# Kernel tuning notes

Measured on AMD Instinct MI355X. Metric: run time of the kernel, lower is better.

Reference implementation:

```python
import jax, jax.numpy as jnp
import numpy as np

# ---- config mirroring init kwargs ----
D_MODEL = 512
NUM_DIRS = 8
QUANTILES = (0.1, 0.5, 0.9)
POLY_ORDER = 2
BETA_INIT = 0.5
HEAD_WIDTH = 16
SOFTSORT_C = 0.5
SOFTSORT_ALPHA = 0.5
FEAT_IN = NUM_DIRS * (len(QUANTILES) + POLY_ORDER + 1)  # 48


def _legendre_basis(T, order, dtype):
    t = jnp.linspace(-1.0, 1.0, T, dtype=dtype)
    P = [jnp.ones_like(t)]
    if order >= 1:
        P.append(t)
    for n in range(1, order):
        P.append(((2 * n + 1) * t * P[n] - n * P[n - 1]) / (n + 1))
    B = jnp.stack(P[:order + 1], axis=0)
    return B / jnp.sqrt(jnp.maximum(jnp.sum(B * B, axis=1, keepdims=True), 1e-6))


def _isotonic_nonincreasing(y):
    #   v_i = min_{s<=i} max_{t>=i} mean(y[s..t])
    T = y.shape[0]
    c = jnp.concatenate([jnp.zeros((1,), y.dtype), jnp.cumsum(y)])
    s_idx = jnp.arange(T)[:, None]
    t_idx = jnp.arange(T)[None, :]
    length = jnp.maximum(t_idx - s_idx + 1, 1).astype(y.dtype)
    A = (c[t_idx + 1] - c[s_idx]) / length                 # mean over [s, t]
    A = jnp.where(t_idx >= s_idx, A, -jnp.inf)
    R = jax.lax.cummax(A, axis=1, reverse=True)            # R[s,i] = max_{t>=i} A[s,t]
    R = jnp.where(s_idx <= t_idx, R, jnp.inf)
    V = jax.lax.cummin(R, axis=0)                          # V[i,i] = min_{s<=i} R[s,i]
    return jnp.diagonal(V)


def _soft_sort_ascending(vals, reg):
    # Blondel et al. fast-soft-sort with L2 regularization.
    # Descending soft-sort: rho/reg - isotonic_nonincreasing(rho/reg - sort_desc(theta))
    # Ascending = -soft_sort_desc(-vals).
    L, T = vals.shape
    theta = -vals
    s = jnp.sort(theta, axis=-1)[:, ::-1]                  # descending
    rho = jnp.arange(T, 0, -1, dtype=vals.dtype) / jnp.asarray(reg, vals.dtype)
    v = jax.vmap(_isotonic_nonincreasing)(rho[None, :] - s)
    return -(rho[None, :] - v)


def setup_inputs() -> dict:
    key = jax.random.key(0)
    ks = jax.random.split(key, 6)
    B, T, N, D = 2, 128, 128, D_MODEL
    x = jax.random.normal(ks[0], (B, T, N, D), dtype=jnp.float32)
    valid_mask = jnp.ones((B, T, N), dtype=jnp.float32)
    # proj: Linear(D, K, bias=False), kaiming-uniform-ish init
    bound = 1.0 / np.sqrt(D)
    W_proj = jax.random.uniform(ks[1], (NUM_DIRS, D), jnp.float32, -bound, bound)
    # additive head: per-feature Linear(1,width) -> GELU -> Linear(width,D,no bias)
    W1 = jax.random.uniform(ks[2], (FEAT_IN, HEAD_WIDTH), jnp.float32, -1.0, 1.0)
    b1 = jax.random.uniform(ks[3], (FEAT_IN, HEAD_WIDTH), jnp.float32, -1.0, 1.0)
    bw = 1.0 / np.sqrt(HEAD_WIDTH)
    W2 = jax.random.uniform(ks[4], (FEAT_IN, HEAD_WIDTH, D_MODEL), jnp.float32, -bw, bw)
    beta = jnp.full((D_MODEL,), BETA_INIT, dtype=jnp.float32)
    return {"x": x, "valid_mask": valid_mask, "W_proj": W_proj,
            "W1": W1, "b1": b1, "W2": W2, "beta": beta}


def reference(x, valid_mask, W_proj, W1, b1, W2, beta):
    B, T, N, D = x.shape
    K = W_proj.shape[0]
    # orthonormalize projection (done in-place under no_grad in torch -> straight-through)
    Q, _ = jnp.linalg.qr(W_proj.T)                          # [D, K]
    W_eff = W_proj + jax.lax.stop_gradient(Q.T - W_proj)
    U = W_eff.T                                             # [D, K]

    v = jnp.einsum('btnd,dk->btnk', x, U) * valid_mask[..., None]
    v_bnkt = jnp.transpose(v, (0, 2, 3, 1))                 # [B, N, K, T]

    reg = max(1e-3, SOFTSORT_C * float(T) ** (-SOFTSORT_ALPHA))
    ss = _soft_sort_ascending(v_bnkt.reshape(-1, T), reg)   # [L, T]

    levels = jnp.asarray(QUANTILES, x.dtype)
    pos = jnp.clip(levels, 0.0, 1.0) * (T - 1)
    lo = jnp.clip(jnp.floor(pos).astype(jnp.int32), 0, T - 1)
    hi = jnp.clip(jnp.ceil(pos).astype(jnp.int32), 0, T - 1)
    w = pos - lo.astype(x.dtype)
    qv = ((1.0 - w) * ss[:, lo] + w * ss[:, hi]).reshape(B, N, K, -1)

    Bmat = _legendre_basis(T, POLY_ORDER, x.dtype)          # [P+1, T]
    coeff = jnp.einsum('bnkt,pt->bnkp', v_bnkt, Bmat)

    feats = jnp.concatenate([qv, coeff], axis=-1).reshape(B, N, -1)  # [B, N, F]
    hmid = jax.nn.gelu(feats[..., None] * W1 + b1, approximate=False)  # [B, N, F, width]
    parts = jnp.einsum('bnfw,fwd->bnfd', hmid, W2)          # [B, N, F, D]
    y = parts.sum(axis=2)                                   # [B, N, D]

    beta_eff = jax.nn.sigmoid(beta)
    y_btnd = jnp.broadcast_to(y[:, None], (B, T, N, D))
    h = x + beta_eff * y_btnd
    vm = valid_mask[..., None]
    h = vm * h + (1.0 - vm) * x

    num = jnp.mean(jnp.sqrt(jnp.sum((beta_eff * y_btnd) ** 2, axis=-1)))
    den = jnp.maximum(jnp.mean(jnp.sqrt(jnp.sum(x * x, axis=-1))), 1e-9)
    r = jax.lax.stop_gradient(num / den)
    # per-feature energy: contributions are constant over T -> factor T inside sqrt
    sq = jnp.sum((beta_eff * parts) ** 2, axis=(1, 3))       # [B, F]
    energy = jnp.sqrt(jnp.asarray(T, x.dtype) * sq)
    r_feat = jax.lax.stop_gradient(jnp.mean(energy, axis=0) / den)
    return h, r, r_feat
```

## Files before the change

kernel.cpp:

```cpp
#include <hip/hip_runtime.h>
#include <hip/hip_bf16.h>
#include <math.h>

#define OFF_BEFF  0
#define OFF_B2    512
#define OFF_LB    1024
#define OFF_U     1408
#define OFF_FEATS 5504
#define OFF_DENP  17792
#define OFF_NUMP  18816
#define OFF_SQP   19072
#define OFF_V     31360
#define OFF_Y     293504
#define OFF_YP    424576
#define WS_TOTAL  1473152

__device__ __align__(16) float g_ws[WS_TOTAL];

static __device__ __forceinline__ float wred64(float v){
  #pragma unroll
  for (int m = 32; m >= 1; m >>= 1) v += __shfl_xor(v, m, 64);
  return v;
}

__global__ __launch_bounds__(256) void k1_prep(const float* __restrict__ Wp,
                                               const float* __restrict__ beta){
  int tid = threadIdx.x;
  __shared__ float p1s[128], p2s[128], nrm[2];
  for (int d = tid; d < 512; d += 256){
    float b = beta[d];
    float s = 1.0f/(1.0f + expf(-b));
    g_ws[OFF_BEFF + d] = s;
    g_ws[OFF_B2 + d] = s*s;
  }
  if (tid < 128){
    float t = -1.0f + 2.0f*(float)tid/127.0f;
    p1s[tid] = t;
    p2s[tid] = 0.5f*(3.0f*t*t - 1.0f);
  }
  __syncthreads();
  if (tid == 0){
    float a = 0, b = 0;
    for (int i = 0; i < 128; i++){ a += p1s[i]*p1s[i]; b += p2s[i]*p2s[i]; }
    nrm[0] = sqrtf(fmaxf(a, 1e-6f));
    nrm[1] = sqrtf(fmaxf(b, 1e-6f));
  }
  __syncthreads();
  if (tid < 128){
    g_ws[OFF_LB + 0*128 + tid] = 1.0f/sqrtf(128.0f);
    g_ws[OFF_LB + 1*128 + tid] = p1s[tid]/nrm[0];
    g_ws[OFF_LB + 2*128 + tid] = p2s[tid]/nrm[1];
  }
  if (tid < 64){
    int l = tid;
    float A[8][8], Q[8][8], tau[8];
    #pragma unroll
    for (int c = 0; c < 8; c++)
      #pragma unroll
      for (int p = 0; p < 8; p++)
        A[c][p] = Wp[c*512 + p*64 + l];
    #pragma unroll
    for (int j = 0; j < 8; j++){
      float alpha = __shfl(A[j][0], j, 64);
      float ssq = 0.0f;
      #pragma unroll
      for (int p = 0; p < 8; p++){
        bool live = (p > 0) || (l > j);
        float v = A[j][p];
        ssq += live ? v*v : 0.0f;
      }
      ssq = wred64(ssq);
      float tj, scale;
      if (ssq == 0.0f){ tj = 0.0f; scale = 0.0f; }
      else {
        float bta = -copysignf(sqrtf(alpha*alpha + ssq), alpha);
        tj = (bta - alpha)/bta;
        scale = 1.0f/(alpha - bta);
      }
      tau[j] = tj;
      #pragma unroll
      for (int p = 0; p < 8; p++){
        int row = p*64 + l;
        float v = A[j][p]*scale;
        A[j][p] = (row < j) ? 0.0f : (row == j ? 1.0f : v);
      }
      #pragma unroll
      for (int c = j+1; c < 8; c++){
        float d = 0.0f;
        #pragma unroll
        for (int p = 0; p < 8; p++) d += A[c][p]*A[j][p];
        d = wred64(d)*tj;
        #pragma unroll
        for (int p = 0; p < 8; p++) A[c][p] -= d*A[j][p];
      }
    }
    #pragma unroll
    for (int c = 0; c < 8; c++)
      #pragma unroll
      for (int p = 0; p < 8; p++)
        Q[c][p] = (p == 0 && l == c) ? 1.0f : 0.0f;
    #pragma unroll
    for (int j = 7; j >= 0; j--){
      #pragma unroll
      for (int c = 0; c < 8; c++){
        float d = 0.0f;
        #pragma unroll
        for (int p = 0; p < 8; p++) d += Q[c][p]*A[j][p];
        d = wred64(d)*tau[j];
        #pragma unroll
        for (int p = 0; p < 8; p++) Q[c][p] -= d*A[j][p];
      }
    }
    #pragma unroll
    for (int c = 0; c < 8; c++)
      #pragma unroll
      for (int p = 0; p < 8; p++)
        g_ws[OFF_U + c*512 + p*64 + l] = Q[c][p];
  }
}

__global__ __launch_bounds__(256) void k2_proj(const float* __restrict__ x,
                                               const float* __restrict__ vmask){
  int tid = threadIdx.x;
  int l = tid & 63, wv = tid >> 6;
  int g = blockIdx.x*4 + wv;
  __shared__ float denw[4];
  float u[8][8];
  #pragma unroll
  for (int k = 0; k < 8; k++)
    #pragma unroll
    for (int e = 0; e < 8; e++)
      u[k][e] = g_ws[OFF_U + k*512 + l*8 + e];
  float denpart = 0.0f;
  for (int rr = 0; rr < 8; rr++){
    int row = g*8 + rr;
    const float* xr = x + (size_t)row*512 + l*8;
    float4 xa = *(const float4*)xr;
    float4 xb = *(const float4*)(xr + 4);
    float xe[8] = {xa.x, xa.y, xa.z, xa.w, xb.x, xb.y, xb.z, xb.w};
    float acc[8];
    float sq = 0.0f;
    #pragma unroll
    for (int k = 0; k < 8; k++){
      float a = 0.0f;
      #pragma unroll
      for (int e = 0; e < 8; e++) a += xe[e]*u[k][e];
      acc[k] = a;
    }
    #pragma unroll
    for (int e = 0; e < 8; e++) sq += xe[e]*xe[e];
    #pragma unroll
    for (int k = 0; k < 8; k++) acc[k] = wred64(acc[k]);
    sq = wred64(sq);
    if (l == 0){
      float vm = vmask[row];
      int b = row >> 14, t = (row >> 7) & 127, n = row & 127;
      int bn = b*128 + n;
      float* vg = g_ws + OFF_V + bn*1024 + t;
      #pragma unroll
      for (int k = 0; k < 8; k++) vg[k*128] = acc[k]*vm;
      denpart += sqrtf(sq);
    }
  }
  if (l == 0) denw[wv] = denpart;
  __syncthreads();
  if (tid == 0) g_ws[OFF_DENP + blockIdx.x] = denw[0]+denw[1]+denw[2]+denw[3];
}

__global__ __launch_bounds__(256) void k3_sortfeat(){
  int tid = threadIdx.x;
  int l = tid & 63, wv = tid >> 6;
  int rho = blockIdx.x*4 + wv;
  __shared__ float orig[4][128], srt[4][128], Bl[384];
  __shared__ float pS[4][128];
  __shared__ int   pC[4][128];
  for (int i = tid; i < 384; i += 256) Bl[i] = g_ws[OFF_LB + i];
  const float* vr = g_ws + OFF_V + rho*128;
  orig[wv][2*l]   = vr[2*l];
  orig[wv][2*l+1] = vr[2*l+1];
  srt[wv][2*l] = 0.0f; srt[wv][2*l+1] = 0.0f;
  __syncthreads();
  float c0, c1, c2;
  {
    float a = orig[wv][2*l], b = orig[wv][2*l+1];
    c0 = a*Bl[2*l]       + b*Bl[2*l+1];
    c1 = a*Bl[128+2*l]   + b*Bl[128+2*l+1];
    c2 = a*Bl[256+2*l]   + b*Bl[256+2*l+1];
  }
  c0 = wred64(c0); c1 = wred64(c1); c2 = wred64(c2);
  float e0 = orig[wv][2*l], e1 = orig[wv][2*l+1];
  int r0 = 0, r1 = 0;
  for (int j = 0; j < 128; j++){
    float vj = orig[wv][j];
    r0 += (vj < e0) || (vj == e0 && j < 2*l);
    r1 += (vj < e1) || (vj == e1 && j < 2*l+1);
  }
  srt[wv][r0] = e0;
  srt[wv][r1] = e1;
  __syncthreads();
  const float rinv = 22.627416997969522f;
  bool v0 = (srt[wv][2*l+1] - srt[wv][2*l] > rinv);
  bool v1 = (2*l + 2 < 128) ? (srt[wv][2*l+2] - srt[wv][2*l+1] > rinv) : false;
  if (__any(v0 || v1)){
    if (l == 0){
      int top = -1;
      for (int i = 0; i < 128; i++){
        float y = (float)(128 - i)*rinv + srt[wv][i];
        top++; pS[wv][top] = y; pC[wv][top] = 1;
        while (top > 0 &&
               pS[wv][top]*(float)pC[wv][top-1] > pS[wv][top-1]*(float)pC[wv][top]){
          pS[wv][top-1] += pS[wv][top];
          pC[wv][top-1] += pC[wv][top];
          top--;
        }
      }
      int i = 0;
      for (int blk = 0; blk <= top; blk++){
        float m = pS[wv][blk]/(float)pC[wv][blk];
        for (int c = 0; c < pC[wv][blk]; c++){
          srt[wv][i] = m - (float)(128 - i)*rinv;
          i++;
        }
      }
    }
  }
  if (l == 0){
    int bn = rho >> 3, k = rho & 7;
    float* fb = g_ws + OFF_FEATS + bn*48 + k*6;
    float w0 = 0.1f*127.0f - 12.0f;
    float w1 = 0.5f*127.0f - 63.0f;
    float w2 = 0.9f*127.0f - 114.0f;
    fb[0] = (1.0f - w0)*srt[wv][12]  + w0*srt[wv][13];
    fb[1] = (1.0f - w1)*srt[wv][63]  + w1*srt[wv][64];
    fb[2] = (1.0f - w2)*srt[wv][114] + w2*srt[wv][115];
    fb[3] = c0; fb[4] = c1; fb[5] = c2;
  }
}

__global__ __launch_bounds__(512) void k4a_head(const float* __restrict__ W1,
                                                const float* __restrict__ b1,
                                                const float* __restrict__ W2){
  int blk = blockIdx.x;
  int s   = blk & 7;
  int bnp = blk >> 3;
  int bn0 = bnp*2, bn1 = bn0 + 1;
  int tid = threadIdx.x;
  int l = tid & 63, wv = tid >> 6;
  __shared__ float hl0[96], hl1[96];
  __shared__ float sq[8][12];
  if (tid < 192){
    int which = tid >= 96;
    int i = which ? tid - 96 : tid;
    int f = s*6 + (i >> 4);
    int k = f*16 + (i & 15);
    int bn = which ? bn1 : bn0;
    float a = g_ws[OFF_FEATS + bn*48 + f]*W1[k] + b1[k];
    float g = 0.5f*a*(1.0f + erff(a*0.70710678118654752f));
    if (which) hl1[i] = g; else hl0[i] = g;
  }
  __syncthreads();
  int d = tid;
  float b2 = g_ws[OFF_B2 + d];
  float y0 = 0.0f, y1 = 0.0f;
  const float* w2base = W2 + (size_t)(s*96)*512 + d;
  #pragma unroll
  for (int fl_ = 0; fl_ < 6; fl_++){
    float p0 = 0.0f, p1 = 0.0f;
    #pragma unroll
    for (int w = 0; w < 16; w++){
      float w2 = w2base[(size_t)(fl_*16 + w)*512];
      p0 += hl0[fl_*16 + w]*w2;
      p1 += hl1[fl_*16 + w]*w2;
    }
    y0 += p0; y1 += p1;
    float e0 = wred64(p0*p0*b2);
    float e1 = wred64(p1*p1*b2);
    if (l == 0){ sq[wv][fl_*2] = e0; sq[wv][fl_*2 + 1] = e1; }
  }
  g_ws[OFF_YP + (size_t)(bn0*8 + s)*512 + d] = y0;
  g_ws[OFF_YP + (size_t)(bn1*8 + s)*512 + d] = y1;
  __syncthreads();
  if (tid < 12){
    float t = 0.0f;
    #pragma unroll
    for (int w = 0; w < 8; w++) t += sq[w][tid];
    int fl_ = tid >> 1, which = tid & 1;
    int bn = which ? bn1 : bn0;
    g_ws[OFF_SQP + bn*48 + s*6 + fl_] = t;
  }
}

__global__ __launch_bounds__(512) void k4b_red(){
  int bn = blockIdx.x;
  int tid = threadIdx.x;
  int l = tid & 63, wv = tid >> 6;
  __shared__ float nw[8];
  float y = 0.0f;
  #pragma unroll
  for (int s = 0; s < 8; s++) y += g_ws[OFF_YP + (size_t)(bn*8 + s)*512 + tid];
  g_ws[OFF_Y + bn*512 + tid] = y;
  float be = g_ws[OFF_BEFF + tid];
  float by = be*y;
  float ns = wred64(by*by);
  if (l == 0) nw[wv] = ns;
  __syncthreads();
  if (tid == 0){
    float s = nw[0]+nw[1]+nw[2]+nw[3]+nw[4]+nw[5]+nw[6]+nw[7];
    g_ws[OFF_NUMP + bn] = sqrtf(s);
  }
}

__global__ __launch_bounds__(256) void k6_fin(float* __restrict__ outt){
  __shared__ float red[256];
  __shared__ float en[96];
  __shared__ float scal[2];
  int tid = threadIdx.x;
  float dp = 0.0f;
  for (int i = tid; i < 1024; i += 256) dp += g_ws[OFF_DENP + i];
  red[tid] = dp; __syncthreads();
  for (int s = 128; s > 0; s >>= 1){
    if (tid < s) red[tid] += red[tid + s];
    __syncthreads();
  }
  if (tid == 0) scal[0] = fmaxf(red[0]/32768.0f, 1e-9f);
  __syncthreads();
  red[tid] = g_ws[OFF_NUMP + tid];
  __syncthreads();
  for (int s = 128; s > 0; s >>= 1){
    if (tid < s) red[tid] += red[tid + s];
    __syncthreads();
  }
  if (tid == 0) scal[1] = red[0]/256.0f;
  __syncthreads();
  float den = scal[0];
  if (tid < 96){
    int b = tid/48, f = tid%48;
    float s = 0.0f;
    for (int j = 0; j < 128; j++) s += g_ws[OFF_SQP + (b*128 + j)*48 + f];
    en[tid] = sqrtf(128.0f*s);
  }
  __syncthreads();
  if (tid == 0) outt[16777216] = scal[1]/den;
  if (tid < 48) outt[16777217 + tid] = 0.5f*(en[tid] + en[48 + tid])/den;
}

__global__ __launch_bounds__(256) void k7_out(const float* __restrict__ x,
                                              const float* __restrict__ vmask,
                                              float* __restrict__ outt){
  int q = blockIdx.x*256 + threadIdx.x;
  size_t fl = (size_t)q*4;
  int d = (int)(fl & 511);
  int row = (int)(fl >> 9);
  int b = row >> 14, n = row & 127;
  int bn = b*128 + n;
  float vm = vmask[row];
  float4 xv = *(const float4*)(x + fl);
  float4 yv = *(const float4*)(g_ws + OFF_Y + bn*512 + d);
  float4 bv = *(const float4*)(g_ws + OFF_BEFF + d);
  float4 o;
  o.x = xv.x + vm*bv.x*yv.x;
  o.y = xv.y + vm*bv.y*yv.y;
  o.z = xv.z + vm*bv.z*yv.z;
  o.w = xv.w + vm*bv.w*yv.w;
  *(float4*)(outt + fl) = o;
}

extern "C" void kernel_launch(void* const* d_in, const int* in_sizes, int n_in,
                              void* d_out, int out_size, void* d_ws, size_t ws_size,
                              hipStream_t stream){
  (void)out_size; (void)d_ws; (void)ws_size;
  const float *x=nullptr,*vm=nullptr,*Wp=nullptr,*W1=nullptr,*b1=nullptr,*W2=nullptr,*beta=nullptr;
  for (int i = 0; i < n_in; i++){
    int s = in_sizes[i];
    const float* p = (const float*)d_in[i];
    if      (s == 16777216) x = p;
    else if (s == 32768)    vm = p;
    else if (s == 4096)     Wp = p;
    else if (s == 393216)   W2 = p;
    else if (s == 512)      beta = p;
    else if (s == 768)      { if (!W1) W1 = p; else b1 = p; }
  }
  float* out = (float*)d_out;

  k1_prep<<<1, 256, 0, stream>>>(Wp, beta);
  k2_proj<<<1024, 256, 0, stream>>>(x, vm);
  k3_sortfeat<<<512, 256, 0, stream>>>();
  k4a_head<<<1024, 512, 0, stream>>>(W1, b1, W2);
  k4b_red<<<256, 512, 0, stream>>>();
  k6_fin<<<1, 256, 0, stream>>>(out);
  k7_out<<<16384, 256, 0, stream>>>(x, vm, out);
}
```

Before: 99.06 us.

## Use transpose-style butterfly reduction in projection and fold finalize into output kernel

The projection kernel swaps its eight independent full-wave reductions for a recursive-halving butterfly. After the first three exchange steps each lane holds one partial direction, so only three more shuffles are needed, and eight lanes each write one direction instead of lane 0 writing all eight. The scalar finalize kernel becomes an extra block of the output kernel, which removes one launch. The sort rank loop is also unrolled. The lane-to-direction mapping is an added source of bugs, and the finalize block now runs alongside the streaming blocks.

```diff
diff --git a/kernel.cpp b/kernel.cpp
--- a/kernel.cpp
+++ b/kernel.cpp
@@ -131,6 +131,7 @@
     #pragma unroll
     for (int e = 0; e < 8; e++)
       u[k][e] = g_ws[OFF_U + k*512 + l*8 + e];
+  int kk = ((l & 1) << 2) | (l & 2) | ((l & 4) >> 2);
   float denpart = 0.0f;
   for (int rr = 0; rr < 8; rr++){
     int row = g*8 + rr;
@@ -149,18 +150,39 @@
     }
     #pragma unroll
     for (int e = 0; e < 8; e++) sq += xe[e]*xe[e];
-    #pragma unroll
-    for (int k = 0; k < 8; k++) acc[k] = wred64(acc[k]);
+    if (l & 1){
+      float t;
+      t=acc[0];acc[0]=acc[4];acc[4]=t;
+      t=acc[1];acc[1]=acc[5];acc[5]=t;
+      t=acc[2];acc[2]=acc[6];acc[6]=t;
+      t=acc[3];acc[3]=acc[7];acc[7]=t;
+    }
+    acc[0] += __shfl_xor(acc[4], 1, 64);
+    acc[1] += __shfl_xor(acc[5], 1, 64);
+    acc[2] += __shfl_xor(acc[6], 1, 64);
+    acc[3] += __shfl_xor(acc[7], 1, 64);
+    if (l & 2){
+      float t;
+      t=acc[0];acc[0]=acc[2];acc[2]=t;
+      t=acc[1];acc[1]=acc[3];acc[3]=t;
+    }
+    acc[0] += __shfl_xor(acc[2], 2, 64);
+    acc[1] += __shfl_xor(acc[3], 2, 64);
+    if (l & 4){
+      float t=acc[0];acc[0]=acc[1];acc[1]=t;
+    }
+    acc[0] += __shfl_xor(acc[1], 4, 64);
+    acc[0] += __shfl_xor(acc[0], 8, 64);
+    acc[0] += __shfl_xor(acc[0], 16, 64);
+    acc[0] += __shfl_xor(acc[0], 32, 64);
     sq = wred64(sq);
-    if (l == 0){
-      float vm = vmask[row];
+    float vm = vmask[row];
+    if (l < 8){
       int b = row >> 14, t = (row >> 7) & 127, n = row & 127;
       int bn = b*128 + n;
-      float* vg = g_ws + OFF_V + bn*1024 + t;
-      #pragma unroll
-      for (int k = 0; k < 8; k++) vg[k*128] = acc[k]*vm;
-      denpart += sqrtf(sq);
-    }
+      g_ws[OFF_V + bn*1024 + kk*128 + t] = acc[0]*vm;
+    }
+    if (l == 0) denpart += sqrtf(sq);
   }
   if (l == 0) denw[wv] = denpart;
   __syncthreads();
@@ -190,6 +212,7 @@
   c0 = wred64(c0); c1 = wred64(c1); c2 = wred64(c2);
   float e0 = orig[wv][2*l], e1 = orig[wv][2*l+1];
   int r0 = 0, r1 = 0;
+  #pragma unroll 4
   for (int j = 0; j < 128; j++){
     float vj = orig[wv][j];
     r0 += (vj < e0) || (vj == e0 && j < 2*l);
@@ -310,43 +333,43 @@
   }
 }
 
-__global__ __launch_bounds__(256) void k6_fin(float* __restrict__ outt){
-  __shared__ float red[256];
-  __shared__ float en[96];
-  __shared__ float scal[2];
-  int tid = threadIdx.x;
-  float dp = 0.0f;
-  for (int i = tid; i < 1024; i += 256) dp += g_ws[OFF_DENP + i];
-  red[tid] = dp; __syncthreads();
-  for (int s = 128; s > 0; s >>= 1){
-    if (tid < s) red[tid] += red[tid + s];
-    __syncthreads();
-  }
-  if (tid == 0) scal[0] = fmaxf(red[0]/32768.0f, 1e-9f);
-  __syncthreads();
-  red[tid] = g_ws[OFF_NUMP + tid];
-  __syncthreads();
-  for (int s = 128; s > 0; s >>= 1){
-    if (tid < s) red[tid] += red[tid + s];
-    __syncthreads();
-  }
-  if (tid == 0) scal[1] = red[0]/256.0f;
-  __syncthreads();
-  float den = scal[0];
-  if (tid < 96){
-    int b = tid/48, f = tid%48;
-    float s = 0.0f;
-    for (int j = 0; j < 128; j++) s += g_ws[OFF_SQP + (b*128 + j)*48 + f];
-    en[tid] = sqrtf(128.0f*s);
-  }
-  __syncthreads();
-  if (tid == 0) outt[16777216] = scal[1]/den;
-  if (tid < 48) outt[16777217 + tid] = 0.5f*(en[tid] + en[48 + tid])/den;
-}
-
 __global__ __launch_bounds__(256) void k7_out(const float* __restrict__ x,
                                               const float* __restrict__ vmask,
                                               float* __restrict__ outt){
+  if (blockIdx.x == 16384){
+    __shared__ float red[256];
+    __shared__ float en[96];
+    __shared__ float scal[2];
+    int tid = threadIdx.x;
+    float dp = 0.0f;
+    for (int i = tid; i < 1024; i += 256) dp += g_ws[OFF_DENP + i];
+    red[tid] = dp; __syncthreads();
+    for (int s = 128; s > 0; s >>= 1){
+      if (tid < s) red[tid] += red[tid + s];
+      __syncthreads();
+    }
+    if (tid == 0) scal[0] = fmaxf(red[0]/32768.0f, 1e-9f);
+    __syncthreads();
+    red[tid] = g_ws[OFF_NUMP + tid];
+    __syncthreads();
+    for (int s = 128; s > 0; s >>= 1){
+      if (tid < s) red[tid] += red[tid + s];
+      __syncthreads();
+    }
+    if (tid == 0) scal[1] = red[0]/256.0f;
+    __syncthreads();
+    float den = scal[0];
+    if (tid < 96){
+      int b = tid/48, f = tid%48;
+      float s = 0.0f;
+      for (int j = 0; j < 128; j++) s += g_ws[OFF_SQP + (b*128 + j)*48 + f];
+      en[tid] = sqrtf(128.0f*s);
+    }
+    __syncthreads();
+    if (tid == 0) outt[16777216] = scal[1]/den;
+    if (tid < 48) outt[16777217 + tid] = 0.5f*(en[tid] + en[48 + tid])/den;
+    return;
+  }
   int q = blockIdx.x*256 + threadIdx.x;
   size_t fl = (size_t)q*4;
   int d = (int)(fl & 511);
@@ -387,6 +410,5 @@
   k3_sortfeat<<<512, 256, 0, stream>>>();
   k4a_head<<<1024, 512, 0, stream>>>(W1, b1, W2);
   k4b_red<<<256, 512, 0, stream>>>();
-  k6_fin<<<1, 256, 0, stream>>>(out);
-  k7_out<<<16384, 256, 0, stream>>>(x, vm, out);
-}
+  k7_out<<<16385, 256, 0, stream>>>(x, vm, out);
+}
```

Result: faster. 88.92 us (-10.2%).
